# Performance work log

Measured on AMD Instinct MI355X. Metric: run time of the kernel, lower is better.

## Reference

```python
import jax, jax.numpy as jnp
import numpy as np

B, T, D, H, L = 2, 2048, 2048, 16, 64
HD = D // H  # 128
EPS = 1e-5


def setup_inputs() -> dict:
    key = jax.random.key(0)
    ks = jax.random.split(key, 16)
    s = 0.02
    inp = {
        'x': jax.random.normal(ks[0], (B, T, D), jnp.float32),
        'mask': jnp.tril(jnp.ones((T, T), dtype=bool)),
        'ln_w': jnp.ones((D,), jnp.float32),
        'ln_b': jnp.zeros((D,), jnp.float32),
        'wq': jax.random.normal(ks[1], (D, D), jnp.float32) * s,
        'bq': jnp.zeros((D,), jnp.float32),
        'wk': jax.random.normal(ks[2], (D, D), jnp.float32) * s,
        'bk': jnp.zeros((D,), jnp.float32),
        'wv': jax.random.normal(ks[3], (D, D), jnp.float32) * s,
        'bv': jnp.zeros((D,), jnp.float32),
        'wo': jax.random.normal(ks[4], (D, D), jnp.float32) * s,
        'bo': jnp.zeros((D,), jnp.float32),
        'wcq': jax.random.normal(ks[5], (HD, L), jnp.float32) * s,
        'bcq': jnp.zeros((L,), jnp.float32),
        'wck': jax.random.normal(ks[6], (HD, L), jnp.float32) * s,
        'bck': jnp.zeros((L,), jnp.float32),
        'wcv': jax.random.normal(ks[7], (HD, L), jnp.float32) * s,
        'bcv': jnp.zeros((L,), jnp.float32),
        'wd': jax.random.normal(ks[8], (L, HD), jnp.float32) * s,
        'bd': jnp.zeros((HD,), jnp.float32),
    }
    # standard RoPE frequency table: theta_i = 10000^{-2i/HD}
    inv_freq = 1.0 / (10000.0 ** (jnp.arange(0, HD, 2, dtype=jnp.float32) / HD))
    ang = jnp.arange(T, dtype=jnp.float32)[:, None] * inv_freq[None, :]  # [T, HD/2]
    inp['freqs_cos'] = jnp.cos(ang)
    inp['freqs_sin'] = jnp.sin(ang)
    return inp


def _rope(x, cos, sin):
    # x: [B,T,H,HD]; cos/sin: [T, HD/2]; interleaved (even=real, odd=imag)
    xr, xi = x[..., 0::2], x[..., 1::2]
    c = cos[None, :, None, :]
    sn = sin[None, :, None, :]
    out_r = xr * c - xi * sn
    out_i = xr * sn + xi * c
    return jnp.stack([out_r, out_i], axis=-1).reshape(x.shape)


def reference(x, mask, freqs_cos, freqs_sin, ln_w, ln_b, wq, bq, wk, bk, wv, bv,
              wo, bo, wcq, bcq, wck, bck, wcv, bcv, wd, bd):
    # LayerNorm
    mu = jnp.mean(x, axis=-1, keepdims=True)
    var = jnp.mean(jnp.square(x - mu), axis=-1, keepdims=True)
    xn = (x - mu) / jnp.sqrt(var + EPS) * ln_w + ln_b

    q = (xn @ wq + bq).reshape(B, T, H, HD)
    k = (xn @ wk + bk).reshape(B, T, H, HD)
    v = (xn @ wv + bv).reshape(B, T, H, HD)

    q, k = _rope(q, freqs_cos, freqs_sin), _rope(k, freqs_cos, freqs_sin)

    # compress each head to the latent dim
    q_lat = q @ wcq + bcq  # [B,T,H,L]
    k_lat = k @ wck + bck
    v_lat = v @ wcv + bcv

    scale = 1.0 / np.sqrt(L).astype(np.float32)
    scores = jnp.einsum('bqhl,bkhl->bhqk', q_lat, k_lat) * scale  # [B,H,T,T]
    additive = jnp.where(mask, 0.0, -1e9).astype(scores.dtype)  # bool mask -> additive
    scores = scores + additive[None, None, :, :]
    attn = jax.nn.softmax(scores, axis=-1)

    out = jnp.einsum('bhqk,bkhl->bqhl', attn, v_lat)  # [B,T,H,L]
    out = (out @ wd + bd).reshape(B, T, D)  # decompress to head_dim, merge heads
    return out @ wo + bo
```

## Files before the change

kernel.cpp:

```cpp
#include <hip/hip_runtime.h>
#include <hip/hip_bf16.h>
#include <stdint.h>

#define BB 2
#define TB 2048
#define DB 2048
#define HB 16
#define HDB 128
#define LB 64
#define MB 4096

typedef __hip_bfloat16 bf16;
typedef __attribute__((ext_vector_type(8))) short bf16x8;
typedef __attribute__((ext_vector_type(4))) float f32x4;

#define MFMA_16x16x32 __builtin_amdgcn_mfma_f32_16x16x32_bf16

typedef __attribute__((address_space(3))) void lds_t;
typedef const __attribute__((address_space(1))) void gvm_t;

static __device__ __forceinline__ float bf2f(bf16 h) { return __bfloat162float(h); }
static __device__ __forceinline__ bf16 f2bf(float f) { return __float2bfloat16(f); }
union BV8 { bf16x8 v; bf16 e[8]; };

#define SWZC(r) (((r) ^ ((r) >> 3)) & 7)

__device__ void do_ln(const float* __restrict__ x, const float* __restrict__ g,
                      const float* __restrict__ be, bf16* __restrict__ xn,
                      int row, int tid, char* sm) {
  float* red = (float*)sm;
  const float4* xr = (const float4*)(x + (size_t)row * DB);
  float4 a = xr[2 * tid], b = xr[2 * tid + 1];
  float s = a.x + a.y + a.z + a.w + b.x + b.y + b.z + b.w;
  float s2 = a.x * a.x + a.y * a.y + a.z * a.z + a.w * a.w +
             b.x * b.x + b.y * b.y + b.z * b.z + b.w * b.w;
  for (int off = 32; off > 0; off >>= 1) {
    s += __shfl_down(s, off);
    s2 += __shfl_down(s2, off);
  }
  int w = tid >> 6, lane = tid & 63;
  if (lane == 0) { red[w] = s; red[4 + w] = s2; }
  __syncthreads();
  s = red[0] + red[1] + red[2] + red[3];
  s2 = red[4] + red[5] + red[6] + red[7];
  float mu = s * (1.f / DB);
  float var = s2 * (1.f / DB) - mu * mu;
  float rstd = rsqrtf(var + 1e-5f);
  const float4* gw = (const float4*)g;
  const float4* bb = (const float4*)be;
  float4 g0 = gw[2 * tid], g1 = gw[2 * tid + 1];
  float4 b0 = bb[2 * tid], b1 = bb[2 * tid + 1];
  BV8 u;
  u.e[0] = f2bf((a.x - mu) * rstd * g0.x + b0.x);
  u.e[1] = f2bf((a.y - mu) * rstd * g0.y + b0.y);
  u.e[2] = f2bf((a.z - mu) * rstd * g0.z + b0.z);
  u.e[3] = f2bf((a.w - mu) * rstd * g0.w + b0.w);
  u.e[4] = f2bf((b.x - mu) * rstd * g1.x + b1.x);
  u.e[5] = f2bf((b.y - mu) * rstd * g1.y + b1.y);
  u.e[6] = f2bf((b.z - mu) * rstd * g1.z + b1.z);
  u.e[7] = f2bf((b.w - mu) * rstd * g1.w + b1.w);
  *(bf16x8*)(xn + (size_t)row * DB + tid * 8) = u.v;
}

__device__ void do_wconv(const float* __restrict__ W, bf16* __restrict__ Wt,
                         int bx, int by, int tid, char* sm) {
  float(*t)[33] = (float(*)[33])sm;
  int c0 = bx * 32, r0 = by * 32;
  int tx = tid & 31, ty = tid >> 5;
  for (int p = 0; p < 4; ++p)
    t[ty + 8 * p][tx] = W[(size_t)(r0 + ty + 8 * p) * DB + c0 + tx];
  __syncthreads();
  for (int p = 0; p < 4; ++p)
    Wt[(size_t)(c0 + ty + 8 * p) * DB + r0 + tx] = f2bf(t[tx][ty + 8 * p]);
}

__device__ void do_fold_v(const float* __restrict__ wv, const float* __restrict__ wcv,
                          bf16* __restrict__ BtV, int bx, int h, int tid, char* sm) {
  float(*wvs)[36] = (float(*)[36])sm;
  int k0 = bx * 128;
  int l = tid & 63, ks = tid >> 6;
  float acc[32];
#pragma unroll
  for (int i = 0; i < 32; ++i) acc[i] = 0.f;
  for (int dc = 0; dc < 128; dc += 32) {
    __syncthreads();
    for (int i = tid; i < 128 * 32; i += 256) {
      int kk = i >> 5, dd = i & 31;
      wvs[kk][dd] = wv[(size_t)(k0 + kk) * DB + h * 128 + dc + dd];
    }
    __syncthreads();
    float wr[32];
#pragma unroll
    for (int dd = 0; dd < 32; ++dd) wr[dd] = wcv[(dc + dd) * 64 + l];
#pragma unroll
    for (int i = 0; i < 32; ++i) {
      const float4* row = (const float4*)&wvs[ks * 32 + i][0];
#pragma unroll
      for (int d4 = 0; d4 < 8; ++d4) {
        float4 w4 = row[d4];
        acc[i] += w4.x * wr[d4 * 4] + w4.y * wr[d4 * 4 + 1] +
                  w4.z * wr[d4 * 4 + 2] + w4.w * wr[d4 * 4 + 3];
      }
    }
  }
  bf16* dst = BtV + (size_t)(h * 64 + l) * DB + k0 + ks * 32;
#pragma unroll
  for (int i8 = 0; i8 < 4; ++i8) {
    BV8 u;
#pragma unroll
    for (int j = 0; j < 8; ++j) u.e[j] = f2bf(acc[i8 * 8 + j]);
    *(bf16x8*)(dst + i8 * 8) = u.v;
  }
}

__device__ void do_fold_o(const float* __restrict__ wo, const float* __restrict__ wd,
                          bf16* __restrict__ BtO, int bx, int h, int tid, char* sm) {
  float(*wos)[132] = (float(*)[132])sm;
  int n0 = bx * 128;
  int l = tid & 63, ns = tid >> 6;
  float acc[32];
#pragma unroll
  for (int i = 0; i < 32; ++i) acc[i] = 0.f;
  for (int dc = 0; dc < 128; dc += 32) {
    __syncthreads();
    for (int i = tid; i < 32 * 128; i += 256) {
      int dd = i >> 7, nn = i & 127;
      wos[dd][nn] = wo[(size_t)(h * 128 + dc + dd) * DB + n0 + nn];
    }
    __syncthreads();
    float wr[32];
#pragma unroll
    for (int d4 = 0; d4 < 8; ++d4) {
      float4 w4 = *(const float4*)&wd[l * 128 + dc + d4 * 4];
      wr[d4 * 4] = w4.x; wr[d4 * 4 + 1] = w4.y;
      wr[d4 * 4 + 2] = w4.z; wr[d4 * 4 + 3] = w4.w;
    }
#pragma unroll
    for (int dd = 0; dd < 32; ++dd) {
      float w = wr[dd];
      const float4* row = (const float4*)&wos[dd][ns * 32];
#pragma unroll
      for (int i4 = 0; i4 < 8; ++i4) {
        float4 a4 = row[i4];
        acc[i4 * 4 + 0] += a4.x * w; acc[i4 * 4 + 1] += a4.y * w;
        acc[i4 * 4 + 2] += a4.z * w; acc[i4 * 4 + 3] += a4.w * w;
      }
    }
  }
#pragma unroll
  for (int i = 0; i < 32; ++i)
    BtO[(size_t)(n0 + ns * 32 + i) * 1024 + h * 64 + l] = f2bf(acc[i]);
}

__global__ __launch_bounds__(256) void prep_kernel(
    const float* __restrict__ x, const float* __restrict__ ln_w,
    const float* __restrict__ ln_b, bf16* __restrict__ xn,
    const float* __restrict__ wq, const float* __restrict__ wk,
    bf16* __restrict__ wqkT,
    const float* __restrict__ wv, const float* __restrict__ wcv,
    bf16* __restrict__ BtV,
    const float* __restrict__ wo, const float* __restrict__ wd,
    bf16* __restrict__ BtO,
    const float* __restrict__ bv, const float* __restrict__ bcv,
    float* __restrict__ bvlat,
    const float* __restrict__ bd, const float* __restrict__ bo,
    float* __restrict__ bo2) {
  __shared__ __align__(16) char sm[18432];
  int b = blockIdx.x, tid = threadIdx.x;
  if (b < 4096) {
    do_ln(x, ln_w, ln_b, xn, b, tid, sm);
  } else if (b < 8192) {
    int bb = b - 4096;
    do_wconv(wq, wqkT, bb & 63, bb >> 6, tid, sm);
  } else if (b < 12288) {
    int bb = b - 8192;
    do_wconv(wk, wqkT + (size_t)2048 * 2048, bb & 63, bb >> 6, tid, sm);
  } else if (b < 12544) {
    int bb = b - 12288;
    do_fold_v(wv, wcv, BtV, bb & 15, bb >> 4, tid, sm);
  } else if (b < 12800) {
    int bb = b - 12544;
    do_fold_o(wo, wd, BtO, bb & 15, bb >> 4, tid, sm);
  } else if (b < 12804) {
    int j = (b - 12800) * 256 + tid;
    int h = j >> 6, l = j & 63;
    float s = bcv[l];
    for (int d = 0; d < 128; ++d) s += bv[h * 128 + d] * wcv[d * 64 + l];
    bvlat[j] = s;
  } else {
    float(*red)[64] = (float(*)[64])sm;
    int nl = tid & 63, ks = tid >> 6;
    int n = (b - 12804) * 64 + nl;
    float s = 0.f;
    for (int k = ks * 512; k < ks * 512 + 512; ++k)
      s += bd[k & 127] * wo[(size_t)k * DB + n];
    red[ks][nl] = s;
    __syncthreads();
    if (ks == 0) bo2[n] = bo[n] + red[0][nl] + red[1][nl] + red[2][nl] + red[3][nl];
  }
}

__global__ __launch_bounds__(256) void gemm_qkv_kernel(
    const bf16* __restrict__ A, const bf16* __restrict__ wqkT,
    const bf16* __restrict__ BtV,
    const float* __restrict__ bq, const float* __restrict__ bk,
    const float* __restrict__ bvl,
    const float* __restrict__ wcq, const float* __restrict__ wck,
    const float* __restrict__ bcq, const float* __restrict__ bck,
    bf16* __restrict__ qlat, bf16* __restrict__ klat, bf16* __restrict__ vlatT,
    const float* __restrict__ fcos, const float* __restrict__ fsin) {
  constexpr int K = DB;
  __shared__ __align__(16) char smem[49152];
  bf16* As = (bf16*)smem;
  bf16* Bs = (bf16*)(smem + 8192);
  bf16* Qt = (bf16*)smem;
  bf16* Wt = (bf16*)(smem + 32768);
  int tid = threadIdx.x;
  int bid = blockIdx.x;
  int j = (bid & 7) * 160 + (bid >> 3);
  int mt = j / 40, nt = j - mt * 40;
  int m0 = mt * 128, n0 = nt * 128;
  int w = tid >> 6, l = tid & 63;
  int wr = w >> 1, wc = w & 1;
  int lrow = l & 15, lk = (l >> 4) * 8, ck = l >> 4;
  const bf16* Bsrc = (n0 < 4096) ? (wqkT + (size_t)n0 * K)
                                 : (BtV + (size_t)(n0 - 4096) * K);
  int sel = n0 >> 11;

  if (sel < 2) {
    const float* wcp = sel == 0 ? wcq : wck;
    for (int i = tid; i < 8192; i += 256) {
      int d = i >> 6, jj = i & 63;
      Wt[jj * 128 + (((d >> 3) ^ (jj & 7)) * 8) + (d & 7)] = f2bf(wcp[d * 64 + jj]);
    }
  }

  f32x4 zero4 = {0.f, 0.f, 0.f, 0.f};
  f32x4 acc[4][4];
  for (int m = 0; m < 4; ++m)
    for (int n = 0; n < 4; ++n) acc[m][n] = zero4;

  for (int kk = 0; kk < K / 32; ++kk) {
    int k0 = kk * 32;
    __syncthreads();
#pragma unroll
    for (int i = 0; i < 2; ++i) {
      int c = i * 256 + tid;
      int r = c >> 2, cc = c & 3;
      int cb = i * 256 + (tid & ~63);
      __builtin_amdgcn_global_load_lds(
          (gvm_t*)&A[(size_t)(m0 + r) * K + k0 + cc * 8], (lds_t*)&As[cb * 8], 16, 0, 0);
      __builtin_amdgcn_global_load_lds(
          (gvm_t*)&Bsrc[(size_t)r * K + k0 + cc * 8], (lds_t*)&Bs[cb * 8], 16, 0, 0);
    }
    __syncthreads();
    bf16x8 af[4], bfr[4];
    for (int m = 0; m < 4; ++m)
      af[m] = *(bf16x8*)&As[(wr * 64 + m * 16 + lrow) * 32 + lk];
    for (int n = 0; n < 4; ++n)
      bfr[n] = *(bf16x8*)&Bs[(wc * 64 + n * 16 + lrow) * 32 + lk];
    for (int m = 0; m < 4; ++m)
      for (int n = 0; n < 4; ++n)
        acc[m][n] = MFMA_16x16x32(af[m], bfr[n], acc[m][n], 0, 0, 0);
  }

  int rg = 4 * (l >> 4), cl = l & 15;
  if (sel == 2) {
    for (int mf = 0; mf < 4; ++mf) {
      int rowb = m0 + wr * 64 + mf * 16 + rg;
      for (int nf = 0; nf < 4; ++nf) {
        int col = n0 + wc * 64 + nf * 16 + cl;
        int colV = col - 4096;
        float bv_ = bvl[colV];
        size_t vbase = ((size_t)((rowb >> 11) * HB + (colV >> 6)) * 64 + (colV & 63)) * TB
                       + (rowb & (TB - 1));
        for (int r = 0; r < 4; ++r)
          vlatT[vbase + r] = f2bf(acc[mf][nf][r] + bv_);
      }
    }
    return;
  }

  const float* bias = sel == 0 ? bq : bk;
  __syncthreads();
  for (int mf = 0; mf < 4; ++mf) {
    int rowb = m0 + wr * 64 + mf * 16 + rg;
    int rl0 = wr * 64 + mf * 16 + rg;
    for (int nf = 0; nf < 4; ++nf) {
      int col = n0 + wc * 64 + nf * 16 + cl;
      int colL = col & 2047;
      int cloc = wc * 64 + nf * 16 + cl;
      float bv_ = bias[colL];
      for (int r = 0; r < 4; ++r) {
        int rr = rowb + r;
        float v = acc[mf][nf][r] + bv_;
        float pv = __shfl_xor(v, 1);
        int t = rr & (TB - 1);
        int pi = (col & 127) >> 1;
        float c = fcos[t * 64 + pi], sn = fsin[t * 64 + pi];
        v = (col & 1) ? (pv * sn + v * c) : (v * c - pv * sn);
        int rl = rl0 + r;
        Qt[rl * 128 + ((((cloc >> 3) ^ (rl & 7)) * 8) + (cloc & 7))] = f2bf(v);
      }
    }
  }
  __syncthreads();
  f32x4 pacc[2][4];
#pragma unroll
  for (int mi = 0; mi < 2; ++mi)
#pragma unroll
    for (int nf = 0; nf < 4; ++nf) pacc[mi][nf] = zero4;
#pragma unroll
  for (int kc = 0; kc < 4; ++kc) {
    bf16x8 aq[2], bw[4];
#pragma unroll
    for (int mi = 0; mi < 2; ++mi) {
      int row = w * 32 + mi * 16 + lrow;
      aq[mi] = *(bf16x8*)&Qt[row * 128 + (((kc * 4 + ck) ^ (row & 7)) * 8)];
    }
#pragma unroll
    for (int nf = 0; nf < 4; ++nf) {
      int jrow = nf * 16 + lrow;
      bw[nf] = *(bf16x8*)&Wt[jrow * 128 + (((kc * 4 + ck) ^ (jrow & 7)) * 8)];
    }
#pragma unroll
    for (int mi = 0; mi < 2; ++mi)
#pragma unroll
      for (int nf = 0; nf < 4; ++nf)
        pacc[mi][nf] = MFMA_16x16x32(aq[mi], bw[nf], pacc[mi][nf], 0, 0, 0);
  }
  int head = (n0 & 2047) >> 7;
  const float* bias2 = sel == 0 ? bcq : bck;
  bf16* outp = sel == 0 ? qlat : klat;
#pragma unroll
  for (int mi = 0; mi < 2; ++mi)
#pragma unroll
    for (int nf = 0; nf < 4; ++nf) {
      int colj = nf * 16 + cl;
      float b2 = bias2[colj];
#pragma unroll
      for (int r = 0; r < 4; ++r) {
        int roG = m0 + w * 32 + mi * 16 + rg + r;
        outp[((size_t)roG * HB + head) * 64 + colj] = f2bf(pacc[mi][nf][r] + b2);
      }
    }
}

__global__ __launch_bounds__(256) void gemm_out_kernel(
    const bf16* __restrict__ A, const bf16* __restrict__ Bt,
    const float* __restrict__ bias, float* __restrict__ Cout) {
  constexpr int K = 1024, N = DB;
  __shared__ __align__(16) bf16 As[128 * 32];
  __shared__ __align__(16) bf16 Bs[128 * 32];
  int tid = threadIdx.x;
  int bid = blockIdx.x;
  int j = (bid & 7) * 64 + (bid >> 3);
  int mt = j >> 4, nt = j & 15;
  int m0 = mt * 128, n0 = nt * 128;
  int w = tid >> 6, l = tid & 63;
  int wr = w >> 1, wc = w & 1;
  int lrow = l & 15, lk = (l >> 4) * 8;

  f32x4 zero4 = {0.f, 0.f, 0.f, 0.f};
  f32x4 acc[4][4];
  for (int m = 0; m < 4; ++m)
    for (int n = 0; n < 4; ++n) acc[m][n] = zero4;

  for (int kk = 0; kk < K / 32; ++kk) {
    int k0 = kk * 32;
    __syncthreads();
#pragma unroll
    for (int i = 0; i < 2; ++i) {
      int c = i * 256 + tid;
      int r = c >> 2, cc = c & 3;
      int cb = i * 256 + (tid & ~63);
      __builtin_amdgcn_global_load_lds(
          (gvm_t*)&A[(size_t)(m0 + r) * K + k0 + cc * 8], (lds_t*)&As[cb * 8], 16, 0, 0);
      __builtin_amdgcn_global_load_lds(
          (gvm_t*)&Bt[(size_t)(n0 + r) * K + k0 + cc * 8], (lds_t*)&Bs[cb * 8], 16, 0, 0);
    }
    __syncthreads();
    bf16x8 af[4], bfr[4];
    for (int m = 0; m < 4; ++m)
      af[m] = *(bf16x8*)&As[(wr * 64 + m * 16 + lrow) * 32 + lk];
    for (int n = 0; n < 4; ++n)
      bfr[n] = *(bf16x8*)&Bs[(wc * 64 + n * 16 + lrow) * 32 + lk];
    for (int m = 0; m < 4; ++m)
      for (int n = 0; n < 4; ++n)
        acc[m][n] = MFMA_16x16x32(af[m], bfr[n], acc[m][n], 0, 0, 0);
  }

  int rg = 4 * (l >> 4), cl = l & 15;
  for (int m = 0; m < 4; ++m) {
    int rowb = m0 + wr * 64 + m * 16 + rg;
    for (int n = 0; n < 4; ++n) {
      int col = n0 + wc * 64 + n * 16 + cl;
      float bv = bias[col];
      for (int r = 0; r < 4; ++r)
        Cout[(size_t)(rowb + r) * N + col] = acc[m][n][r] + bv;
    }
  }
}

__global__ __launch_bounds__(256) void attn_kernel(const bf16* __restrict__ qlat,
                                                   const bf16* __restrict__ klat,
                                                   const bf16* __restrict__ vlatT,
                                                   bf16* __restrict__ aout) {
  int tid = threadIdx.x, w = tid >> 6, l = tid & 63;
  int job = ((int)blockIdx.x & 7) * 64 + ((int)blockIdx.x >> 3);
  int bh = job >> 4, pair = job & 15;
  int h = bh & 15, b = bh >> 4;
  int lrow = l & 15, ck = l >> 4, hi4 = l >> 4;
  __shared__ __align__(16) bf16 Ks[2][64 * 64];
  __shared__ __align__(16) bf16 VsT[2][64 * 64];
  __shared__ __align__(16) bf16 Ps[4][16 * 64];
  f32x4 zero4 = {0.f, 0.f, 0.f, 0.f};

#define ASTAGE(buf, kv0)                                                          \
  {                                                                               \
    _Pragma("unroll") for (int i = 0; i < 2; ++i) {                               \
      int c = i * 256 + tid;                                                      \
      int row = c >> 3, ch = c & 7;                                               \
      int dst = (c & ~63) * 8;                                                    \
      __builtin_amdgcn_global_load_lds(                                           \
          (gvm_t*)(klat + ((size_t)(b * TB + (kv0) + row) * HB + h) * LB +        \
                   ((ch ^ SWZC(row)) * 8)),                                       \
          (lds_t*)&Ks[buf][dst], 16, 0, 0);                                       \
      __builtin_amdgcn_global_load_lds(                                           \
          (gvm_t*)(vlatT + ((size_t)bh * 64 + row) * TB + (kv0) +                 \
                   ((ch ^ SWZC(row)) * 8)),                                       \
          (lds_t*)&VsT[buf][dst], 16, 0, 0);                                      \
    }                                                                             \
  }

  for (int half = 0; half < 2; ++half) {
    int tile = half ? pair : 31 - pair;
    int q0 = tile * 64;
    const bf16* qp = qlat + ((size_t)(b * TB + q0 + w * 16 + lrow) * HB + h) * LB;
    bf16x8 qf0 = *(const bf16x8*)(qp + ck * 8);
    bf16x8 qf1 = *(const bf16x8*)(qp + 32 + ck * 8);
    float mr[4], lsum[4];
    f32x4 o[4];
    for (int r = 0; r < 4; ++r) { mr[r] = -1e30f; lsum[r] = 0.f; }
    for (int n = 0; n < 4; ++n) o[n] = zero4;

    __syncthreads();
    ASTAGE(0, 0)
    asm volatile("s_waitcnt vmcnt(0)");
    __syncthreads();

    for (int kt = 0; kt <= tile; ++kt) {
      int cur = kt & 1;
      int kv0 = kt * 64;
      if (kt < tile) ASTAGE(cur ^ 1, kv0 + 64)
      f32x4 s[4];
      __builtin_amdgcn_s_setprio(1);
#pragma unroll
      for (int kg = 0; kg < 4; ++kg) {
        int row = kg * 16 + lrow;
        int sw = SWZC(row);
        bf16x8 kf0 = *(bf16x8*)&Ks[cur][row * 64 + ((ck ^ sw) * 8)];
        bf16x8 kf1 = *(bf16x8*)&Ks[cur][row * 64 + (((ck + 4) ^ sw) * 8)];
        f32x4 a = zero4;
        a = MFMA_16x16x32(qf0, kf0, a, 0, 0, 0);
        a = MFMA_16x16x32(qf1, kf1, a, 0, 0, 0);
        s[kg] = a;
      }
      __builtin_amdgcn_s_setprio(0);
      float sc[4][4];
      bool diag = (kt == tile);
#pragma unroll
      for (int kg = 0; kg < 4; ++kg)
#pragma unroll
        for (int r = 0; r < 4; ++r) {
          float v = s[kg][r] * 0.125f;
          if (diag) {
            int kvg = kv0 + kg * 16 + lrow;
            int qr = q0 + w * 16 + 4 * hi4 + r;
            if (kvg > qr) v = -1e30f;
          }
          sc[kg][r] = v;
        }
      float rm[4], f[4], psum[4];
#pragma unroll
      for (int r = 0; r < 4; ++r)
        rm[r] = fmaxf(fmaxf(sc[0][r], sc[1][r]), fmaxf(sc[2][r], sc[3][r]));
      for (int off = 8; off > 0; off >>= 1)
#pragma unroll
        for (int r = 0; r < 4; ++r) rm[r] = fmaxf(rm[r], __shfl_xor(rm[r], off));
#pragma unroll
      for (int r = 0; r < 4; ++r) {
        float mn = fmaxf(mr[r], rm[r]);
        f[r] = __expf(mr[r] - mn);
        mr[r] = mn;
      }
#pragma unroll
      for (int kg = 0; kg < 4; ++kg)
#pragma unroll
        for (int r = 0; r < 4; ++r) sc[kg][r] = __expf(sc[kg][r] - mr[r]);
#pragma unroll
      for (int r = 0; r < 4; ++r)
        psum[r] = sc[0][r] + sc[1][r] + sc[2][r] + sc[3][r];
      for (int off = 8; off > 0; off >>= 1)
#pragma unroll
        for (int r = 0; r < 4; ++r) psum[r] += __shfl_xor(psum[r], off);
#pragma unroll
      for (int r = 0; r < 4; ++r) lsum[r] = lsum[r] * f[r] + psum[r];
#pragma unroll
      for (int n = 0; n < 4; ++n) {
        f32x4 t = o[n];
        t[0] *= f[0]; t[1] *= f[1]; t[2] *= f[2]; t[3] *= f[3];
        o[n] = t;
      }
#pragma unroll
      for (int r = 0; r < 4; ++r) {
        int rq = 4 * hi4 + r;
        int sw8 = SWZC(rq) << 3;
#pragma unroll
        for (int kg = 0; kg < 4; ++kg)
          Ps[w][rq * 64 + ((kg * 16 + lrow) ^ sw8)] = f2bf(sc[kg][r]);
      }
      int swp = SWZC(lrow);
      bf16x8 pa0 = *(bf16x8*)&Ps[w][lrow * 64 + ((ck ^ swp) * 8)];
      bf16x8 pa1 = *(bf16x8*)&Ps[w][lrow * 64 + (((ck + 4) ^ swp) * 8)];
      __builtin_amdgcn_s_setprio(1);
#pragma unroll
      for (int n = 0; n < 4; ++n) {
        int row = n * 16 + lrow;
        int sw = SWZC(row);
        bf16x8 vf0 = *(bf16x8*)&VsT[cur][row * 64 + ((ck ^ sw) * 8)];
        bf16x8 vf1 = *(bf16x8*)&VsT[cur][row * 64 + (((ck + 4) ^ sw) * 8)];
        o[n] = MFMA_16x16x32(pa0, vf0, o[n], 0, 0, 0);
        o[n] = MFMA_16x16x32(pa1, vf1, o[n], 0, 0, 0);
      }
      __builtin_amdgcn_s_setprio(0);
      asm volatile("s_waitcnt vmcnt(0)");
      __syncthreads();
    }
    float inv[4];
#pragma unroll
    for (int r = 0; r < 4; ++r) inv[r] = 1.f / lsum[r];
#pragma unroll
    for (int n = 0; n < 4; ++n)
#pragma unroll
      for (int r = 0; r < 4; ++r) {
        size_t row = (size_t)b * TB + q0 + w * 16 + 4 * hi4 + r;
        aout[(row * HB + h) * LB + n * 16 + lrow] = f2bf(o[n][r] * inv[r]);
      }
  }
#undef ASTAGE
}

extern "C" void kernel_launch(void* const* d_in, const int* in_sizes, int n_in,
                              void* d_out, int out_size, void* d_ws, size_t ws_size,
                              hipStream_t stream) {
  const float* x    = (const float*)d_in[0];
  const float* ln_w = (const float*)d_in[2];
  const float* ln_b = (const float*)d_in[3];
  const float* wq   = (const float*)d_in[4];
  const float* bq   = (const float*)d_in[5];
  const float* wk   = (const float*)d_in[6];
  const float* bk   = (const float*)d_in[7];
  const float* wv   = (const float*)d_in[8];
  const float* bv   = (const float*)d_in[9];
  const float* wo   = (const float*)d_in[10];
  const float* bo   = (const float*)d_in[11];
  const float* wcq  = (const float*)d_in[12];
  const float* bcq  = (const float*)d_in[13];
  const float* wck  = (const float*)d_in[14];
  const float* bck  = (const float*)d_in[15];
  const float* wcv  = (const float*)d_in[16];
  const float* bcv  = (const float*)d_in[17];
  const float* wd   = (const float*)d_in[18];
  const float* bd   = (const float*)d_in[19];
  const float* fcos = (const float*)d_in[20];
  const float* fsin = (const float*)d_in[21];

  char* ws = (char*)d_ws;
  bf16*  xn    = (bf16*)(ws);
  bf16*  wqkT  = (bf16*)(ws + 16777216);
  bf16*  BtV   = (bf16*)(ws + 33554432);
  bf16*  BtO   = (bf16*)(ws + 37748736);
  bf16*  qlat  = (bf16*)(ws + 41943040);
  bf16*  klat  = (bf16*)(ws + 58720256);
  bf16*  vlatT = (bf16*)(ws + 75497472);
  float* bvlat = (float*)(ws + 83886080);
  float* bo2   = (float*)(ws + 83890176);
  bf16*  aoutp = wqkT;

  prep_kernel<<<12836, 256, 0, stream>>>(
      x, ln_w, ln_b, xn, wq, wk, wqkT, wv, wcv, BtV, wo, wd, BtO,
      bv, bcv, bvlat, bd, bo, bo2);

  gemm_qkv_kernel<<<1280, 256, 0, stream>>>(
      xn, wqkT, BtV, bq, bk, bvlat, wcq, wck, bcq, bck,
      qlat, klat, vlatT, fcos, fsin);

  attn_kernel<<<512, 256, 0, stream>>>(qlat, klat, vlatT, aoutp);

  gemm_out_kernel<<<512, 256, 0, stream>>>(aoutp, BtO, bo2, (float*)d_out);
}
```

Before: 314.5 us.

## Transpose attention score MFMA, use lazy softmax rescale, drop XCD-swizzled grid mapping

The attention kernel now computes scores as K·Qᵀ, so each lane holds one query row. The row max and sum then need only two cross-lane shuffles instead of four-step butterflies over four rows, and P can be written to LDS as packed 4-element vectors. Online-softmax rescaling of the output accumulator is skipped unless some row's max grows by more than 8, which trades exact running-max tracking for fewer exp and multiply ops. Separately, both GEMM kernels replace the XCD-aware block-index remapping with a plain 2D grid, which may change L2 locality across chiplets.

After: 283.4 us (median of 2 runs). 1.11x faster.

```diff
diff --git a/kernel.cpp b/kernel.cpp
--- a/kernel.cpp
+++ b/kernel.cpp
@@ -22,6 +22,7 @@
 static __device__ __forceinline__ float bf2f(bf16 h) { return __bfloat162float(h); }
 static __device__ __forceinline__ bf16 f2bf(float f) { return __float2bfloat16(f); }
 union BV8 { bf16x8 v; bf16 e[8]; };
+union BV4 { ushort4 v; bf16 e[4]; };
 
 #define SWZC(r) (((r) ^ ((r) >> 3)) & 7)
 
@@ -216,10 +217,7 @@
   bf16* Qt = (bf16*)smem;
   bf16* Wt = (bf16*)(smem + 32768);
   int tid = threadIdx.x;
-  int bid = blockIdx.x;
-  int j = (bid & 7) * 160 + (bid >> 3);
-  int mt = j / 40, nt = j - mt * 40;
-  int m0 = mt * 128, n0 = nt * 128;
+  int m0 = blockIdx.y * 128, n0 = blockIdx.x * 128;
   int w = tid >> 6, l = tid & 63;
   int wr = w >> 1, wc = w & 1;
   int lrow = l & 15, lk = (l >> 4) * 8, ck = l >> 4;
@@ -353,10 +351,7 @@
   __shared__ __align__(16) bf16 As[128 * 32];
   __shared__ __align__(16) bf16 Bs[128 * 32];
   int tid = threadIdx.x;
-  int bid = blockIdx.x;
-  int j = (bid & 7) * 64 + (bid >> 3);
-  int mt = j >> 4, nt = j & 15;
-  int m0 = mt * 128, n0 = nt * 128;
+  int m0 = blockIdx.y * 128, n0 = blockIdx.x * 128;
   int w = tid >> 6, l = tid & 63;
   int wr = w >> 1, wc = w & 1;
   int lrow = l & 15, lk = (l >> 4) * 8;
@@ -439,10 +434,11 @@
     const bf16* qp = qlat + ((size_t)(b * TB + q0 + w * 16 + lrow) * HB + h) * LB;
     bf16x8 qf0 = *(const bf16x8*)(qp + ck * 8);
     bf16x8 qf1 = *(const bf16x8*)(qp + 32 + ck * 8);
-    float mr[4], lsum[4];
+    float mr = -1e30f, lsum = 0.f;
     f32x4 o[4];
-    for (int r = 0; r < 4; ++r) { mr[r] = -1e30f; lsum[r] = 0.f; }
     for (int n = 0; n < 4; ++n) o[n] = zero4;
+    int qr = q0 + w * 16 + lrow;
+    int swq = SWZC(lrow);
 
     __syncthreads();
     ASTAGE(0, 0)
@@ -462,8 +458,8 @@
         bf16x8 kf0 = *(bf16x8*)&Ks[cur][row * 64 + ((ck ^ sw) * 8)];
         bf16x8 kf1 = *(bf16x8*)&Ks[cur][row * 64 + (((ck + 4) ^ sw) * 8)];
         f32x4 a = zero4;
-        a = MFMA_16x16x32(qf0, kf0, a, 0, 0, 0);
-        a = MFMA_16x16x32(qf1, kf1, a, 0, 0, 0);
+        a = MFMA_16x16x32(kf0, qf0, a, 0, 0, 0);
+        a = MFMA_16x16x32(kf1, qf1, a, 0, 0, 0);
         s[kg] = a;
       }
       __builtin_amdgcn_s_setprio(0);
@@ -475,54 +471,55 @@
         for (int r = 0; r < 4; ++r) {
           float v = s[kg][r] * 0.125f;
           if (diag) {
-            int kvg = kv0 + kg * 16 + lrow;
-            int qr = q0 + w * 16 + 4 * hi4 + r;
+            int kvg = kv0 + kg * 16 + hi4 * 4 + r;
             if (kvg > qr) v = -1e30f;
           }
           sc[kg][r] = v;
         }
-      float rm[4], f[4], psum[4];
-#pragma unroll
-      for (int r = 0; r < 4; ++r)
-        rm[r] = fmaxf(fmaxf(sc[0][r], sc[1][r]), fmaxf(sc[2][r], sc[3][r]));
-      for (int off = 8; off > 0; off >>= 1)
-#pragma unroll
-        for (int r = 0; r < 4; ++r) rm[r] = fmaxf(rm[r], __shfl_xor(rm[r], off));
-#pragma unroll
-      for (int r = 0; r < 4; ++r) {
-        float mn = fmaxf(mr[r], rm[r]);
-        f[r] = __expf(mr[r] - mn);
-        mr[r] = mn;
-      }
+      float rm = sc[0][0];
 #pragma unroll
       for (int kg = 0; kg < 4; ++kg)
 #pragma unroll
-        for (int r = 0; r < 4; ++r) sc[kg][r] = __expf(sc[kg][r] - mr[r]);
-#pragma unroll
-      for (int r = 0; r < 4; ++r)
-        psum[r] = sc[0][r] + sc[1][r] + sc[2][r] + sc[3][r];
-      for (int off = 8; off > 0; off >>= 1)
-#pragma unroll
-        for (int r = 0; r < 4; ++r) psum[r] += __shfl_xor(psum[r], off);
-#pragma unroll
-      for (int r = 0; r < 4; ++r) lsum[r] = lsum[r] * f[r] + psum[r];
-#pragma unroll
-      for (int n = 0; n < 4; ++n) {
-        f32x4 t = o[n];
-        t[0] *= f[0]; t[1] *= f[1]; t[2] *= f[2]; t[3] *= f[3];
-        o[n] = t;
-      }
-#pragma unroll
-      for (int r = 0; r < 4; ++r) {
-        int rq = 4 * hi4 + r;
-        int sw8 = SWZC(rq) << 3;
-#pragma unroll
-        for (int kg = 0; kg < 4; ++kg)
-          Ps[w][rq * 64 + ((kg * 16 + lrow) ^ sw8)] = f2bf(sc[kg][r]);
-      }
-      int swp = SWZC(lrow);
-      bf16x8 pa0 = *(bf16x8*)&Ps[w][lrow * 64 + ((ck ^ swp) * 8)];
-      bf16x8 pa1 = *(bf16x8*)&Ps[w][lrow * 64 + (((ck + 4) ^ swp) * 8)];
+        for (int r = 0; r < 4; ++r) rm = fmaxf(rm, sc[kg][r]);
+      rm = fmaxf(rm, __shfl_xor(rm, 16));
+      rm = fmaxf(rm, __shfl_xor(rm, 32));
+      bool resc = __any(rm > mr + 8.f);
+      float f = 1.f;
+      if (resc) {
+        float mn = fmaxf(mr, rm);
+        f = __expf(mr - mn);
+        mr = mn;
+      }
+#pragma unroll
+      for (int kg = 0; kg < 4; ++kg)
+#pragma unroll
+        for (int r = 0; r < 4; ++r) sc[kg][r] = __expf(sc[kg][r] - mr);
+      float ps = 0.f;
+#pragma unroll
+      for (int kg = 0; kg < 4; ++kg)
+#pragma unroll
+        for (int r = 0; r < 4; ++r) ps += sc[kg][r];
+      ps += __shfl_xor(ps, 16);
+      ps += __shfl_xor(ps, 32);
+      lsum = lsum * f + ps;
+      if (resc) {
+#pragma unroll
+        for (int r = 0; r < 4; ++r) {
+          float fo = __shfl(f, hi4 * 4 + r, 64);
+#pragma unroll
+          for (int n = 0; n < 4; ++n) o[n][r] *= fo;
+        }
+      }
+#pragma unroll
+      for (int kg = 0; kg < 4; ++kg) {
+        BV4 p4;
+#pragma unroll
+        for (int r = 0; r < 4; ++r) p4.e[r] = f2bf(sc[kg][r]);
+        int kvb = kg * 16 + hi4 * 4;
+        *(ushort4*)&Ps[w][lrow * 64 + (((kvb >> 3) ^ swq) * 8) + (kvb & 7)] = p4.v;
+      }
+      bf16x8 pa0 = *(bf16x8*)&Ps[w][lrow * 64 + ((ck ^ swq) * 8)];
+      bf16x8 pa1 = *(bf16x8*)&Ps[w][lrow * 64 + (((ck + 4) ^ swq) * 8)];
       __builtin_amdgcn_s_setprio(1);
 #pragma unroll
       for (int n = 0; n < 4; ++n) {
@@ -539,7 +536,10 @@
     }
     float inv[4];
 #pragma unroll
-    for (int r = 0; r < 4; ++r) inv[r] = 1.f / lsum[r];
+    for (int r = 0; r < 4; ++r) {
+      float lo = __shfl(lsum, hi4 * 4 + r, 64);
+      inv[r] = 1.f / lo;
+    }
 #pragma unroll
     for (int n = 0; n < 4; ++n)
 #pragma unroll
@@ -592,11 +592,11 @@
       x, ln_w, ln_b, xn, wq, wk, wqkT, wv, wcv, BtV, wo, wd, BtO,
       bv, bcv, bvlat, bd, bo, bo2);
 
-  gemm_qkv_kernel<<<1280, 256, 0, stream>>>(
+  gemm_qkv_kernel<<<dim3(40, 32), 256, 0, stream>>>(
       xn, wqkT, BtV, bq, bk, bvlat, wcq, wck, bcq, bck,
       qlat, klat, vlatT, fcos, fsin);
 
   attn_kernel<<<512, 256, 0, stream>>>(qlat, klat, vlatT, aoutp);
 
-  gemm_out_kernel<<<512, 256, 0, stream>>>(aoutp, BtO, bo2, (float*)d_out);
-}
+  gemm_out_kernel<<<dim3(16, 32), 256, 0, stream>>>(aoutp, BtO, bo2, (float*)d_out);
+}
```
